# Kernel tuning notes

Hardware: AMD Instinct MI355X
Metric: run time of the kernel (lower is better)

## Reference

```python
import jax, jax.numpy as jnp
import numpy as np
import math

H = 300
B = 2048
SEG = 48
N = B * SEG

def _gru_direction(x_seq, h0, w_ih, w_hh, b_ih, b_hh, reverse):
    # x_seq: [L, B, H]; h0: [B, H]; w_ih/w_hh: [3H, H]; b_ih/b_hh: [3H]
    xp = jnp.einsum('lbh,gh->lbg', x_seq, w_ih) + b_ih  # precompute input projections [L,B,3H]
    def step(h, xp_t):
        hp = h @ w_hh.T + b_hh
        xr, xz, xn = jnp.split(xp_t, 3, axis=-1)
        hr, hz, hn = jnp.split(hp, 3, axis=-1)
        r = jax.nn.sigmoid(xr + hr)
        z = jax.nn.sigmoid(xz + hz)
        n = jnp.tanh(xn + r * hn)
        h_new = (1.0 - z) * n + z * h
        return h_new, h_new
    _, ys = jax.lax.scan(step, h0, xp, reverse=reverse)
    return ys  # [L, B, H]

def setup_inputs() -> dict:
    key = jax.random.key(0)
    ks = jax.random.split(key, 12)
    bound = 1.0 / math.sqrt(H)
    u = lambda k, shape: jax.random.uniform(k, shape, jnp.float32, -bound, bound)
    x = jax.random.normal(ks[0], (N, H), jnp.float32)
    batch = jnp.repeat(jnp.arange(B, dtype=jnp.int32), SEG)  # sorted segment ids
    return {
        'x': x,
        'batch': batch,
        'num_moles': B,
        'max_len': SEG,
        'bias': u(ks[1], (H,)),
        'w_ih_f': u(ks[2], (3 * H, H)),
        'w_hh_f': u(ks[3], (3 * H, H)),
        'b_ih_f': u(ks[4], (3 * H,)),
        'b_hh_f': u(ks[5], (3 * H,)),
        'w_ih_b': u(ks[6], (3 * H, H)),
        'w_hh_b': u(ks[7], (3 * H, H)),
        'b_ih_b': u(ks[8], (3 * H,)),
        'b_hh_b': u(ks[9], (3 * H,)),
    }

def reference(x, batch, num_moles, max_len, bias, w_ih_f, w_hh_f, b_ih_f, b_hh_f, w_ih_b, w_hh_b, b_ih_b, b_hh_b):
    n, h = x.shape
    message = jax.nn.relu(x + bias)
    counts = jax.ops.segment_sum(jnp.ones_like(batch), batch, num_segments=num_moles)
    offsets = jnp.cumsum(counts) - counts
    pos = jnp.arange(n, dtype=batch.dtype) - offsets[batch]  # position within molecule
    # ragged -> padded pack [B, L, H]
    padded = jnp.zeros((num_moles, max_len, h), x.dtype).at[batch, pos].set(message)
    # initial hidden = per-molecule max over raw x (same h0 for both directions)
    h0 = jax.ops.segment_max(x, batch, num_segments=num_moles)  # [B, H]
    xs = padded.transpose(1, 0, 2)  # [L, B, H]
    yf = _gru_direction(xs, h0, w_ih_f, w_hh_f, b_ih_f, b_hh_f, reverse=False)
    yb = _gru_direction(xs, h0, w_ih_b, w_hh_b, b_ih_b, b_hh_b, reverse=True)
    y = jnp.concatenate([yf, yb], axis=-1).transpose(1, 0, 2)  # [B, L, 2H]
    return y[batch, pos]  # unpad -> [N, 2H]
```

## Files before the change

kernel.cpp:

```cpp
#include <hip/hip_runtime.h>
#include <hip/hip_bf16.h>

#define H    300
#define KP   320
#define BM   2048
#define SEG  48
#define NTOK (BM*SEG)
#define G    900
#define GP   912
#define NT   57
#define GW   1024
#define XPW  912
#define MOLW 16
#define WGT  1024
#define NPAIR (MOLW*150)
#define PIT  3
#define BKX  64

typedef __attribute__((ext_vector_type(8))) short short8;
typedef __attribute__((ext_vector_type(4))) float f32x4;

__device__ __forceinline__ float lo16(unsigned u) { return __uint_as_float(u << 16); }
__device__ __forceinline__ float hi16(unsigned u) { return __uint_as_float(u & 0xffff0000u); }
__device__ __forceinline__ unsigned short bfb(float f) {
    __hip_bfloat16 b = __float2bfloat16(f);
    return *(unsigned short*)&b;
}
__device__ __forceinline__ void gload16(const void* g, void* l) {
    __builtin_amdgcn_global_load_lds((const __attribute__((address_space(1))) unsigned*)g,
                                     (__attribute__((address_space(3))) unsigned*)l, 16, 0, 0);
}

__global__ void prep_weights(const float* wih_f, const float* whh_f, const float* bih_f,
                             const float* wih_b, const float* whh_b, const float* bih_b,
                             __hip_bfloat16* wih, __hip_bfloat16* whh, float* bih) {
    int idx = blockIdx.x * 256 + threadIdx.x;
    const int wih_n = 2 * GW * KP;
    const int whh_n = 2 * GP * KP;
    if (idx < wih_n) {
        int d = idx / (GW * KP);
        int r = (idx / KP) % GW;
        int k = idx % KP;
        const float* src = d ? wih_b : wih_f;
        float v = (r < G && k < H) ? src[r * H + k] : 0.f;
        wih[idx] = __float2bfloat16(v);
        return;
    }
    idx -= wih_n;
    if (idx < whh_n) {
        int d = idx / (GP * KP);
        int r = (idx / KP) % GP;
        int k = idx % KP;
        const float* src = d ? whh_b : whh_f;
        float v = (r < G && k < H) ? src[r * H + k] : 0.f;
        whh[idx] = __float2bfloat16(v);
        return;
    }
    idx -= whh_n;
    if (idx < 2 * GW) {
        int d = idx / GW;
        int r = idx % GW;
        const float* src = d ? bih_b : bih_f;
        bih[idx] = (r < G) ? src[r] : 0.f;
    }
}

__global__ void prep_msg(const float* x, const float* bias, __hip_bfloat16* msg) {
    int idx = blockIdx.x * 256 + threadIdx.x;
    if (idx >= NTOK * KP) return;
    int i = idx / KP, k = idx % KP;
    float v = 0.f;
    if (k < H) {
        v = x[i * H + k] + bias[k];
        v = v > 0.f ? v : 0.f;
    }
    msg[idx] = __float2bfloat16(v);
}

__global__ void h0_kernel(const float* x, float* h0) {
    int m = blockIdx.x;
    for (int c = threadIdx.x; c < H; c += blockDim.x) {
        const float* base = x + (long long)m * SEG * H + c;
        float v = -INFINITY;
        for (int t = 0; t < SEG; t++) v = fmaxf(v, base[t * H]);
        h0[m * H + c] = v;
    }
}

__global__ __launch_bounds__(256) void xp_gemm(const __hip_bfloat16* msg, const __hip_bfloat16* wih,
                                               const float* bih, __hip_bfloat16* xp) {
    int d = blockIdx.z;
    const __hip_bfloat16* A  = msg;
    const __hip_bfloat16* Bw = wih + d * GW * KP;
    const float* bi = bih + d * GW;
    __hip_bfloat16* out = xp + (long long)d * NTOK * XPW;

    __shared__ __hip_bfloat16 sA[128 * BKX];
    __shared__ __hip_bfloat16 sB[128 * BKX];
    const short* sAs = (const short*)sA;
    const short* sBs = (const short*)sB;

    int tid = threadIdx.x;
    int lane = tid & 63, wid = tid >> 6;
    int l15 = lane & 15, quad = lane >> 4;
    int mblk = blockIdx.x * 128, nblk = blockIdx.y * 128;
    int mbase = (wid >> 1) * 64, nbase = (wid & 1) * 64;

    int srow = wid * 32 + (lane >> 3);
    int scc  = (lane & 7) ^ (srow & 7);
    const short* gA0 = (const short*)A  + (long long)(mblk + srow) * KP + scc * 8;
    const short* gB0 = (const short*)Bw + (long long)(nblk + srow) * KP + scc * 8;
    int xsw = (l15 & 7) << 3;

    f32x4 acc[4][4] = {};
    for (int kc = 0; kc < KP / BKX; kc++) {
#pragma unroll
        for (int j = 0; j < 4; j++)
            gload16(gA0 + (long long)j * 8 * KP + kc * BKX, (char*)sA + (wid * 4 + j) * 1024);
#pragma unroll
        for (int j = 0; j < 4; j++)
            gload16(gB0 + (long long)j * 8 * KP + kc * BKX, (char*)sB + (wid * 4 + j) * 1024);
        __syncthreads();

        short8 af[4][2], bf[4][2];
#pragma unroll
        for (int i = 0; i < 4; i++)
#pragma unroll
            for (int kh = 0; kh < 2; kh++)
                af[i][kh] = *(const short8*)(sAs + (mbase + i * 16 + l15) * BKX + ((kh * 32 + quad * 8) ^ xsw));
#pragma unroll
        for (int j = 0; j < 4; j++)
#pragma unroll
            for (int kh = 0; kh < 2; kh++)
                bf[j][kh] = *(const short8*)(sBs + (nbase + j * 16 + l15) * BKX + ((kh * 32 + quad * 8) ^ xsw));
#pragma unroll
        for (int i = 0; i < 4; i++)
#pragma unroll
            for (int j = 0; j < 4; j++) {
                acc[i][j] = __builtin_amdgcn_mfma_f32_16x16x32_bf16(af[i][0], bf[j][0], acc[i][j], 0, 0, 0);
                acc[i][j] = __builtin_amdgcn_mfma_f32_16x16x32_bf16(af[i][1], bf[j][1], acc[i][j], 0, 0, 0);
            }
        __syncthreads();
    }

#pragma unroll
    for (int i = 0; i < 4; i++)
#pragma unroll
        for (int j = 0; j < 4; j++) {
            int col = nblk + nbase + j * 16 + l15;
            if (col < XPW) {
                float bv = bi[col];
#pragma unroll
                for (int r = 0; r < 4; r++) {
                    int row = mblk + mbase + i * 16 + quad * 4 + r;
                    out[(long long)row * XPW + col] = __float2bfloat16(acc[i][j][r] + bv);
                }
            }
        }
}

__global__ __launch_bounds__(WGT, 4) void gru_kernel(const __hip_bfloat16* whh_all, const float* bhh_f,
                                                     const float* bhh_b, const __hip_bfloat16* xp,
                                                     const float* h0, float* out) {
    int grp = blockIdx.x;
    int d   = blockIdx.y;
    const short* Ws = (const short*)(whh_all + d * GP * KP);
    const float* bhh = d ? bhh_b : bhh_f;
    const __hip_bfloat16* xpd = xp + (long long)d * NTOK * XPW;

    int tid = threadIdx.x;
    int lane = tid & 63, wid = tid >> 6;
    int l15 = lane & 15, quad = lane >> 4;

    __shared__ __hip_bfloat16 hB[MOLW * 328];
    __shared__ __hip_bfloat16 hp[MOLW * GP];
    const short* hBs = (const short*)hB;

    int mol0 = grp * MOLW;

    for (int e = tid; e < MOLW * 328; e += WGT) hB[e] = __float2bfloat16(0.f);

    float bvw[4];
#pragma unroll
    for (int k = 0; k < 4; k++) {
        int nt = wid + 16 * k;
        int gc = nt * 16 + l15;
        bvw[k] = (nt < NT && gc < G) ? bhh[gc] : 0.f;
    }
    __syncthreads();

    float hv0[PIT], hv1[PIT];
#pragma unroll
    for (int i = 0; i < PIT; i++) {
        int e2 = tid + i * WGT;
        if (e2 < NPAIR) {
            int m = e2 / 150, c = 2 * (e2 % 150);
            float2 hh = *(const float2*)(h0 + (size_t)(mol0 + m) * H + c);
            hv0[i] = hh.x; hv1[i] = hh.y;
            unsigned pack = ((unsigned)bfb(hh.y) << 16) | bfb(hh.x);
            *(unsigned*)(&hB[m * 328 + c]) = pack;
        }
    }
    __syncthreads();

    for (int t = 0; t < SEG; t++) {
        int tt = d ? (SEG - 1 - t) : t;

        unsigned pr[PIT], pz[PIT], pn[PIT];
#pragma unroll
        for (int i = 0; i < PIT; i++) {
            int e2 = tid + i * WGT;
            if (e2 < NPAIR) {
                int m = e2 / 150, c = 2 * (e2 % 150);
                const __hip_bfloat16* xrow = xpd + ((long long)(mol0 + m) * SEG + tt) * XPW;
                pr[i] = *(const unsigned*)(xrow + c);
                pz[i] = *(const unsigned*)(xrow + c + 300);
                pn[i] = *(const unsigned*)(xrow + c + 600);
            }
        }

        short8 afA[10];
#pragma unroll
        for (int kk = 0; kk < 10; kk++) {
            int koff = kk * 32 + quad * 8;
            afA[kk] = *(const short8*)(hBs + l15 * 328 + koff);
        }

        int k8 = 0;
        for (int nt = wid; nt < NT; nt += 16, k8++) {
            int gcol = nt * 16 + l15;
            const short* bp = Ws + gcol * KP;
            f32x4 acc0 = {0.f, 0.f, 0.f, 0.f};
#pragma unroll
            for (int kk = 0; kk < 10; kk++) {
                short8 b = *(const short8*)(bp + kk * 32 + quad * 8);
                acc0 = __builtin_amdgcn_mfma_f32_16x16x32_bf16(afA[kk], b, acc0, 0, 0, 0);
            }
            float bv = bvw[k8];
#pragma unroll
            for (int r = 0; r < 4; r++)
                hp[(quad * 4 + r) * GP + gcol] = __float2bfloat16(acc0[r] + bv);
        }
        __syncthreads();

#pragma unroll
        for (int i = 0; i < PIT; i++) {
            int e2 = tid + i * WGT;
            if (e2 < NPAIR) {
                int m = e2 / 150, c = 2 * (e2 % 150);
                unsigned hr2 = *(const unsigned*)(&hp[m * GP + c]);
                unsigned hz2 = *(const unsigned*)(&hp[m * GP + c + 300]);
                unsigned hn2 = *(const unsigned*)(&hp[m * GP + c + 600]);

                float xr0 = lo16(pr[i]), xr1 = hi16(pr[i]);
                float xz0 = lo16(pz[i]), xz1 = hi16(pz[i]);
                float xn0 = lo16(pn[i]), xn1 = hi16(pn[i]);
                float hr0 = lo16(hr2),  hr1 = hi16(hr2);
                float hz0 = lo16(hz2),  hz1 = hi16(hz2);
                float hn0 = lo16(hn2),  hn1 = hi16(hn2);

                float rg0 = 1.f / (1.f + __expf(-(xr0 + hr0)));
                float rg1 = 1.f / (1.f + __expf(-(xr1 + hr1)));
                float zg0 = 1.f / (1.f + __expf(-(xz0 + hz0)));
                float zg1 = 1.f / (1.f + __expf(-(xz1 + hz1)));
                float ni0 = xn0 + rg0 * hn0;
                float ni1 = xn1 + rg1 * hn1;
                float ng0 = 1.f - 2.f / (__expf(2.f * ni0) + 1.f);
                float ng1 = 1.f - 2.f / (__expf(2.f * ni1) + 1.f);
                float h0n = (1.f - zg0) * ng0 + zg0 * hv0[i];
                float h1n = (1.f - zg1) * ng1 + zg1 * hv1[i];
                hv0[i] = h0n; hv1[i] = h1n;

                unsigned pack = ((unsigned)bfb(h1n) << 16) | bfb(h0n);
                *(unsigned*)(&hB[m * 328 + c]) = pack;

                long long tok = (long long)(mol0 + m) * SEG + tt;
                *(float2*)(out + tok * 600 + d * 300 + c) = make_float2(h0n, h1n);
            }
        }
        __syncthreads();
    }
}

extern "C" void kernel_launch(void* const* d_in, const int* in_sizes, int n_in,
                              void* d_out, int out_size, void* d_ws, size_t ws_size,
                              hipStream_t stream) {
    const float* x     = (const float*)d_in[0];
    const float* bias  = (const float*)d_in[4];
    const float* wih_f = (const float*)d_in[5];
    const float* whh_f = (const float*)d_in[6];
    const float* bih_f = (const float*)d_in[7];
    const float* bhh_f = (const float*)d_in[8];
    const float* wih_b = (const float*)d_in[9];
    const float* whh_b = (const float*)d_in[10];
    const float* bih_b = (const float*)d_in[11];
    const float* bhh_b = (const float*)d_in[12];
    float* out = (float*)d_out;

    char* ws = (char*)d_ws;
    __hip_bfloat16* msg = (__hip_bfloat16*)(ws);
    __hip_bfloat16* wih = (__hip_bfloat16*)(ws + 62914560LL);
    __hip_bfloat16* whh = (__hip_bfloat16*)(ws + 64225280LL);
    float*          bih = (float*)         (ws + 65392640LL);
    float*          h0  = (float*)         (ws + 65400832LL);
    __hip_bfloat16* xp  = (__hip_bfloat16*)(ws + 67858432LL);

    hipLaunchKernelGGL(prep_weights, dim3((2*GW*KP + 2*GP*KP + 2*GW + 255) / 256), dim3(256), 0, stream,
                       wih_f, whh_f, bih_f, wih_b, whh_b, bih_b, wih, whh, bih);
    hipLaunchKernelGGL(prep_msg, dim3((NTOK * KP + 255) / 256), dim3(256), 0, stream, x, bias, msg);
    hipLaunchKernelGGL(h0_kernel, dim3(BM), dim3(256), 0, stream, x, h0);
    hipLaunchKernelGGL(xp_gemm, dim3(NTOK / 128, GW / 128, 2), dim3(256), 0, stream, msg, wih, bih, xp);
    hipLaunchKernelGGL(gru_kernel, dim3(BM / MOLW, 2), dim3(WGT), 0, stream, whh, bhh_f, bhh_b, xp, h0, out);
}
```

Baseline: 1.507 ms.

## Software-pipeline W_hh loads across four interleaved MFMA tiles per wave

Each wave now handles all four of its gate-column tiles at once with four independent accumulators. It prefetches the next k-slice of W_hh through inline-asm global loads, placing explicit vmcnt waits and sched barriers around them. The h fragment is streamed from LDS one k-step ahead rather than preloaded in full. This hides global-load latency behind MFMA work and removes the serial per-tile loop, at the cost of more registers, some redundant loads for tiles that do not exist, and fragile hand-placed waitcnt.

```diff
diff --git a/kernel.cpp b/kernel.cpp
--- a/kernel.cpp
+++ b/kernel.cpp
@@ -159,6 +159,9 @@
         }
 }
 
+#define GLD(dst, base, imm) \
+    asm volatile("global_load_dwordx4 %0, %1, off offset:%2" : "=v"(dst) : "v"(base), "n"(imm))
+
 __global__ __launch_bounds__(WGT, 4) void gru_kernel(const __hip_bfloat16* whh_all, const float* bhh_f,
                                                      const float* bhh_b, const __hip_bfloat16* xp,
                                                      const float* h0, float* out) {
@@ -180,10 +183,13 @@
 
     for (int e = tid; e < MOLW * 328; e += WGT) hB[e] = __float2bfloat16(0.f);
 
+    const short* bp4[4];
     float bvw[4];
 #pragma unroll
     for (int k = 0; k < 4; k++) {
         int nt = wid + 16 * k;
+        int ntc = (nt < NT) ? nt : wid;
+        bp4[k] = Ws + (ntc * 16 + l15) * KP + quad * 8;
         int gc = nt * 16 + l15;
         bvw[k] = (nt < NT && gc < G) ? bhh[gc] : 0.f;
     }
@@ -218,28 +224,44 @@
                 pn[i] = *(const unsigned*)(xrow + c + 600);
             }
         }
-
-        short8 afA[10];
+        __builtin_amdgcn_sched_barrier(0);
+
+        f32x4 acc0 = {}, acc1 = {}, acc2 = {}, acc3 = {};
+        short8 bc0, bc1, bc2, bc3, bn0, bn1, bn2, bn3;
+        GLD(bc0, bp4[0], 0); GLD(bc1, bp4[1], 0); GLD(bc2, bp4[2], 0); GLD(bc3, bp4[3], 0);
+        short8 ac = *(const short8*)(hBs + l15 * 328 + quad * 8);
 #pragma unroll
         for (int kk = 0; kk < 10; kk++) {
-            int koff = kk * 32 + quad * 8;
-            afA[kk] = *(const short8*)(hBs + l15 * 328 + koff);
-        }
-
-        int k8 = 0;
-        for (int nt = wid; nt < NT; nt += 16, k8++) {
-            int gcol = nt * 16 + l15;
-            const short* bp = Ws + gcol * KP;
-            f32x4 acc0 = {0.f, 0.f, 0.f, 0.f};
-#pragma unroll
-            for (int kk = 0; kk < 10; kk++) {
-                short8 b = *(const short8*)(bp + kk * 32 + quad * 8);
-                acc0 = __builtin_amdgcn_mfma_f32_16x16x32_bf16(afA[kk], b, acc0, 0, 0, 0);
-            }
-            float bv = bvw[k8];
-#pragma unroll
-            for (int r = 0; r < 4; r++)
-                hp[(quad * 4 + r) * GP + gcol] = __float2bfloat16(acc0[r] + bv);
+            if (kk < 9) {
+                GLD(bn0, bp4[0], (kk + 1) * 64); GLD(bn1, bp4[1], (kk + 1) * 64);
+                GLD(bn2, bp4[2], (kk + 1) * 64); GLD(bn3, bp4[3], (kk + 1) * 64);
+                asm volatile("s_waitcnt vmcnt(4)" ::: "memory");
+            } else {
+                asm volatile("s_waitcnt vmcnt(0)" ::: "memory");
+            }
+            __builtin_amdgcn_sched_barrier(0);
+            short8 an;
+            if (kk < 9) an = *(const short8*)(hBs + l15 * 328 + (kk + 1) * 32 + quad * 8);
+            acc0 = __builtin_amdgcn_mfma_f32_16x16x32_bf16(ac, bc0, acc0, 0, 0, 0);
+            acc1 = __builtin_amdgcn_mfma_f32_16x16x32_bf16(ac, bc1, acc1, 0, 0, 0);
+            acc2 = __builtin_amdgcn_mfma_f32_16x16x32_bf16(ac, bc2, acc2, 0, 0, 0);
+            acc3 = __builtin_amdgcn_mfma_f32_16x16x32_bf16(ac, bc3, acc3, 0, 0, 0);
+            bc0 = bn0; bc1 = bn1; bc2 = bn2; bc3 = bn3; ac = an;
+        }
+
+        {
+            f32x4 accs[4] = {acc0, acc1, acc2, acc3};
+#pragma unroll
+            for (int k = 0; k < 4; k++) {
+                int nt = wid + 16 * k;
+                if (nt < NT) {
+                    int gcol = nt * 16 + l15;
+                    float bv = bvw[k];
+#pragma unroll
+                    for (int r = 0; r < 4; r++)
+                        hp[(quad * 4 + r) * GP + gcol] = __float2bfloat16(accs[k][r] + bv);
+                }
+            }
         }
         __syncthreads();
 
```

Measured after the change: 1.634 ms. 8.4% more time.
